# Kernel tuning notes

Hardware: AMD Instinct MI355X
Metric: run time of the kernel (lower is better)

The kernel has to match this reference:

```python
import jax, jax.numpy as jnp
import numpy as np

HEADS = 16
EPS = 1e-5

def _ln(t):
    # LayerNorm over last axis, no affine params
    mu = jnp.mean(t, axis=-1, keepdims=True)
    var = jnp.var(t, axis=-1, keepdims=True)
    return (t - mu) / jnp.sqrt(var + EPS)

def setup_inputs() -> dict:
    key = jax.random.key(0)
    ks = jax.random.split(key, 8)
    b, n, dim, mlp_dim = 4, 2048, 1024, 4096
    s = lambda d: 1.0 / np.sqrt(d)
    return {
        "x": jax.random.normal(ks[0], (b, n, dim), dtype=jnp.float32),
        "Wqkv": jax.random.uniform(ks[1], (dim, 3 * dim), jnp.float32, -s(dim), s(dim)),
        "W1": jax.random.uniform(ks[2], (dim, mlp_dim), jnp.float32, -s(dim), s(dim)),
        "b1": jax.random.uniform(ks[3], (mlp_dim,), jnp.float32, -s(dim), s(dim)),
        "W2": jax.random.uniform(ks[4], (mlp_dim, dim), jnp.float32, -s(mlp_dim), s(mlp_dim)),
        "b2": jax.random.uniform(ks[5], (dim,), jnp.float32, -s(mlp_dim), s(mlp_dim)),
        "Wout": jax.random.uniform(ks[6], (dim, dim), jnp.float32, -s(dim), s(dim)),
        "bout": jax.random.uniform(ks[7], (dim,), jnp.float32, -s(dim), s(dim)),
    }

def reference(x, Wqkv, W1, b1, W2, b2, Wout, bout):
    b, n, dim = x.shape
    h = HEADS
    d = dim // h
    scale = dim ** (-0.5)  # NOTE: module scales by full dim, not head_dim
    qkv = x @ Wqkv  # [b, n, 3*dim]
    qkv = qkv.reshape(b, n, 3, h, d).transpose(2, 0, 3, 1, 4)  # [3, b, h, n, d]
    q, k, v = qkv[0], qkv[1], qkv[2]
    q, k = _ln(q), _ln(k)
    dots = jnp.einsum('bhid,bhjd->bhij', q, k) * scale
    attn = jax.nn.softmax(dots, axis=-1)
    attn_v = jnp.einsum('bhij,bhjd->bhid', attn, v)
    attn_v = attn_v.transpose(0, 2, 1, 3).reshape(b, n, dim)
    attn_out = attn_v @ Wout + bout
    parallel = jax.nn.gelu(x @ W1 + b1, approximate=False) @ W2 + b2
    return _ln(attn_out + parallel)
```

## Files before the change

### kernel.cpp

```cpp
#include <hip/hip_runtime.h>

typedef __attribute__((ext_vector_type(8))) short s16x8;
typedef __attribute__((ext_vector_type(4))) short s16x4;
typedef __attribute__((ext_vector_type(4))) float f32x4;
typedef __attribute__((ext_vector_type(16))) float f32x16;
typedef __attribute__((ext_vector_type(2))) unsigned uint2v;

#define DEVINL __device__ __forceinline__

DEVINL float b2f(short u){ return __uint_as_float(((unsigned)(unsigned short)u) << 16); }
DEVINL short f2bf(float f){
  unsigned u = __float_as_uint(f);
  u += 0x7fffu + ((u >> 16) & 1u);
  return (short)(u >> 16);
}
DEVINL unsigned cvtpk(float lo, float hi){
  unsigned r;
  asm("v_cvt_pk_bf16_f32 %0, %1, %2" : "=v"(r) : "v"(lo), "v"(hi));
  return r;
}
DEVINL float max3f(float a, float b, float c){
  float r; asm("v_max3_f32 %0, %1, %2, %3" : "=v"(r) : "v"(a), "v"(b), "v"(c)); return r;
}

#if __has_builtin(__builtin_amdgcn_exp2f)
#define EXP2F __builtin_amdgcn_exp2f
#else
#define EXP2F exp2f
#endif

DEVINL f32x4 mfma32(s16x8 a, s16x8 b, f32x4 c){
  return __builtin_amdgcn_mfma_f32_16x16x32_bf16(a, b, c, 0, 0, 0);
}
DEVINL f32x16 mfma3216(s16x8 a, s16x8 b, f32x16 c){
  return __builtin_amdgcn_mfma_f32_32x32x16_bf16(a, b, c, 0, 0, 0);
}

DEVINL uint2v pl32swap(unsigned a, unsigned b){
#if __has_builtin(__builtin_amdgcn_permlane32_swap)
  return __builtin_amdgcn_permlane32_swap(a, b, false, false);
#else
  asm volatile("v_permlane32_swap_b32 %0, %1" : "+v"(a), "+v"(b));
  uint2v r; r[0] = a; r[1] = b; return r;
#endif
}

typedef const unsigned __attribute__((address_space(1)))* gas1;
typedef unsigned __attribute__((address_space(3)))* las3;
DEVINL void gload16(const short* g, short* l){
  __builtin_amdgcn_global_load_lds((gas1)g, (las3)l, 16, 0, 0);
}

#define CFENCE asm volatile("" ::: "memory")
#define PBAR  do{ CFENCE; __builtin_amdgcn_sched_barrier(0); __builtin_amdgcn_s_barrier(); \
                  __builtin_amdgcn_sched_barrier(0); CFENCE; }while(0)
#define VMW4 asm volatile("s_waitcnt vmcnt(4)" ::: "memory")
#define VMW3 asm volatile("s_waitcnt vmcnt(3)" ::: "memory")
#define VMW0 asm volatile("s_waitcnt vmcnt(0)" ::: "memory")
#define PRIO1 __builtin_amdgcn_s_setprio(1)
#define PRIO0 __builtin_amdgcn_s_setprio(0)

static const int Bc   = 4;
static const int Nc   = 2048;
static const int DIM  = 1024;
static const int Tc   = Bc * Nc;
static const int MLP  = 4096;
static const int D3   = 3072;

static const size_t OFF_XB    = 0;
static const size_t OFF_WQKVT = OFF_XB    + 16777216;
static const size_t OFF_W1T   = OFF_WQKVT + 6291456;
static const size_t OFF_W2T   = OFF_W1T   + 8388608;
static const size_t OFF_WOUTT = OFF_W2T   + 8388608;
static const size_t OFF_QKV   = OFF_WOUTT + 2097152;
static const size_t OFF_QLN   = OFF_QKV   + 50331648;
static const size_t OFF_KLN   = OFF_QLN   + 16777216;
static const size_t OFF_VT    = OFF_KLN   + 16777216;
static const size_t OFF_ATTNV = OFF_VT    + 16777216;
static const size_t OFF_H     = OFF_QKV;
static const size_t OFF_P2    = OFF_KLN;
static const size_t OFF_A2    = OFF_VT;

__global__ __launch_bounds__(256) void conv_x(const float* __restrict__ x, short* __restrict__ xb){
  size_t i = ((size_t)blockIdx.x * 256 + threadIdx.x) * 8;
  f32x4 v0 = *(const f32x4*)(x + i);
  f32x4 v1 = *(const f32x4*)(x + i + 4);
  s16x8 o;
#pragma unroll
  for (int j = 0; j < 4; ++j){ o[j] = f2bf(v0[j]); o[4+j] = f2bf(v1[j]); }
  *(s16x8*)(xb + i) = o;
}

__global__ __launch_bounds__(256) void transpose_conv(const float* __restrict__ W, short* __restrict__ Wt,
                                                      int K, int N){
  __shared__ float tile[32][33];
  int ntx = N >> 5;
  int tx = blockIdx.x % ntx, ty = blockIdx.x / ntx;
  int r = threadIdx.x >> 3, c = (threadIdx.x & 7) * 4;
  f32x4 v = *(const f32x4*)(W + (size_t)(ty*32 + r)*N + tx*32 + c);
  tile[r][c] = v[0]; tile[r][c+1] = v[1]; tile[r][c+2] = v[2]; tile[r][c+3] = v[3];
  __syncthreads();
  s16x4 o;
#pragma unroll
  for (int j = 0; j < 4; ++j) o[j] = f2bf(tile[c+j][r]);
  *(s16x4*)(Wt + (size_t)(tx*32 + r)*K + ty*32 + c) = o;
}

template<int BM, int ACT>
__global__ __launch_bounds__(512, 2) void gemmDP(const short* __restrict__ A, const short* __restrict__ Bt,
                                                 short* __restrict__ C, const float* __restrict__ bias,
                                                 int M, int N, int K){
  constexpr int MREP = BM/32;
  __shared__ short sA0[4096], sA1[4096], sA2[4096], sA3[4096];
  __shared__ short sA4[(BM==256)?4096:4], sA5[(BM==256)?4096:4];
  __shared__ short sA6[(BM==256)?4096:4], sA7[(BM==256)?4096:4];
  __shared__ short sB0[8192], sB1[8192], sB2[8192], sB3[8192];

  const int tid = threadIdx.x;
  const int w = tid >> 6, lane = tid & 63;
  const int lr = lane & 15, g = lane >> 4;
  const int wr = w >> 2, wc = w & 3;
  const int NT = K >> 6;
  const int NIT = NT >> 1;

  const int nbn = N >> 8;
  const int cpx = gridDim.x >> 3;
  const int bid = (int)blockIdx.x;
  const int sw = (bid & 7)*cpx + (bid >> 3);
  const int bm = sw / nbn, bn = sw % nbn;

  const int l2 = lane >> 2;
  const int gsw = ((lane & 3) - ((lane >> 3) & 3)) & 3;
  const int cof = gsw * 8;
  const int qsw8 = ((g + (lr >> 1)) & 3) * 8;

  const size_t arow = (BM==256) ? (size_t)(bm*256 + (w>>2)*128 + (w&3)*16 + l2)
                                : (size_t)(bm*128 + w*16 + l2);
  const short* ap0 = A  + arow*K + cof;
  const short* bp0 = Bt + (size_t)(bn*256 + w*16 + l2)*K + cof;

#define STA_(ARR, T, mh, kk) gload16(ap0 + (size_t)(mh)*64*K + (size_t)(T)*64 + (kk)*32, ARR + w*512)
#define STB_(ARR, T, kk) do{ gload16(bp0 + (size_t)(T)*64 + (kk)*32, ARR + w*512); \
                             gload16(bp0 + (size_t)128*K + (size_t)(T)*64 + (kk)*32, ARR + 4096 + w*512); }while(0)
#define LDA_(ARR, mi) (*(const s16x8*)&ARR[(wr*64 + (mi)*16 + lr)*32 + qsw8])
#define LDB_(ARR, ni) (*(const s16x8*)&ARR[(wc*64 + (ni)*16 + lr)*32 + qsw8])

  f32x4 acc[MREP][4] = {};

#define MMROW(ai, r) \
  acc[r][0]=mfma32(ai,b0,acc[r][0]); acc[r][1]=mfma32(ai,b1,acc[r][1]); \
  acc[r][2]=mfma32(ai,b2,acc[r][2]); acc[r][3]=mfma32(ai,b3,acc[r][3]);
#define RDA4(ARR) { a0=LDA_(ARR,0); a1=LDA_(ARR,1); a2=LDA_(ARR,2); a3=LDA_(ARR,3); }
#define RDB4(ARR) { b0=LDB_(ARR,0); b1=LDB_(ARR,1); b2=LDB_(ARR,2); b3=LDB_(ARR,3); }

  if constexpr (BM==256){
    STA_(sA0,0,0,0); STA_(sA1,0,1,0); STB_(sB0,0,0);
    STA_(sA2,0,0,1); STA_(sA3,0,1,1); STB_(sB1,0,1);
    STA_(sA4,1,0,0); STA_(sA5,1,1,0); STB_(sB2,1,0);
    VMW4;
  } else {
    STA_(sA0,0,0,0); STB_(sB0,0,0);
    STA_(sA1,0,0,1); STB_(sB1,0,1);
    STA_(sA2,1,0,0); STB_(sB2,1,0);
    VMW3;
  }
  PBAR;

  for (int i = 0; i < NIT; ++i){
    const int t = i << 1;
    const bool more = (t + 2 < NT);
    s16x8 a0,a1,a2,a3,b0,b1,b2,b3;

    if constexpr (BM==256){
      RDA4(sA0) RDB4(sB0)
      STA_(sA6, t+1, 0, 1); STA_(sA7, t+1, 1, 1);
      PBAR; PRIO1; MMROW(a0,0) MMROW(a1,1) MMROW(a2,2) MMROW(a3,3) PRIO0; PBAR;
      RDA4(sA1)
      STB_(sB3, t+1, 1);
      PBAR; PRIO1; MMROW(a0,4) MMROW(a1,5) MMROW(a2,6) MMROW(a3,7) PRIO0; PBAR;
      RDA4(sA2) RDB4(sB1)
      if (more){ STA_(sA0, t+2, 0, 0); STA_(sA1, t+2, 1, 0); }
      PBAR; PRIO1; MMROW(a0,0) MMROW(a1,1) MMROW(a2,2) MMROW(a3,3) PRIO0; PBAR;
      RDA4(sA3)
      if (more){ STB_(sB0, t+2, 0); }
      PBAR; PRIO1; MMROW(a0,4) MMROW(a1,5) MMROW(a2,6) MMROW(a3,7) PRIO0;
      if (more){ VMW4; } else { VMW0; }
      PBAR;
      RDA4(sA4) RDB4(sB2)
      if (more){ STA_(sA2, t+2, 0, 1); STA_(sA3, t+2, 1, 1); }
      PBAR; PRIO1; MMROW(a0,0) MMROW(a1,1) MMROW(a2,2) MMROW(a3,3) PRIO0; PBAR;
      RDA4(sA5)
      if (more){ STB_(sB1, t+2, 1); }
      PBAR; PRIO1; MMROW(a0,4) MMROW(a1,5) MMROW(a2,6) MMROW(a3,7) PRIO0; PBAR;
      RDA4(sA6) RDB4(sB3)
      if (more){ STA_(sA4, t+3, 0, 0); STA_(sA5, t+3, 1, 0); }
      PBAR; PRIO1; MMROW(a0,0) MMROW(a1,1) MMROW(a2,2) MMROW(a3,3) PRIO0; PBAR;
      RDA4(sA7)
      if (more){ STB_(sB2, t+3, 0); }
      PBAR; PRIO1; MMROW(a0,4) MMROW(a1,5) MMROW(a2,6) MMROW(a3,7) PRIO0;
      if (more){ VMW4; }
      PBAR;
    } else {
      RDA4(sA0) RDB4(sB0)
      STA_(sA3, t+1, 0, 1); STB_(sB3, t+1, 1);
      PBAR; PRIO1; MMROW(a0,0) MMROW(a1,1) MMROW(a2,2) MMROW(a3,3) PRIO0; PBAR;
      RDA4(sA1) RDB4(sB1)
      if (more){ STA_(sA0, t+2, 0, 0); STB_(sB0, t+2, 0); }
      PBAR; PRIO1; MMROW(a0,0) MMROW(a1,1) MMROW(a2,2) MMROW(a3,3) PRIO0;
      if (more){ VMW3; } else { VMW0; }
      PBAR;
      RDA4(sA2) RDB4(sB2)
      if (more){ STA_(sA1, t+2, 0, 1); STB_(sB1, t+2, 1); }
      PBAR; PRIO1; MMROW(a0,0) MMROW(a1,1) MMROW(a2,2) MMROW(a3,3) PRIO0; PBAR;
      RDA4(sA3) RDB4(sB3)
      if (more){ STA_(sA2, t+3, 0, 0); STB_(sB2, t+3, 0); }
      PBAR; PRIO1; MMROW(a0,0) MMROW(a1,1) MMROW(a2,2) MMROW(a3,3) PRIO0;
      if (more){ VMW3; }
      PBAR;
    }
  }
#undef MMROW
#undef RDA4
#undef RDB4
#undef STA_
#undef STB_
#undef LDA_
#undef LDB_

#pragma unroll
  for (int ni = 0; ni < 4; ++ni){
    const int col = bn*256 + wc*64 + ni*16 + lr;
    const float bv = bias ? bias[col] : 0.f;
#pragma unroll
    for (int a = 0; a < MREP; ++a){
      const int row0 = bm*BM + wr*(BM/2) + a*16 + 4*g;
      f32x4 v = acc[a][ni];
#pragma unroll
      for (int i = 0; i < 4; ++i){
        float val = v[i] + bv;
        if constexpr (ACT) val = 0.5f*val*(1.f + erff(val*0.70710678118f));
        C[(size_t)(row0+i)*N + col] = f2bf(val);
      }
    }
  }
}

__global__ __launch_bounds__(256) void ln_reorg(const short* __restrict__ qkv, short* __restrict__ qln,
                                                short* __restrict__ kln, short* __restrict__ vtb){
  __shared__ short vtile[64*72];
  int bh = blockIdx.x >> 5, tch = blockIdx.x & 31;
  int b = bh >> 4, h = bh & 15;
  int tq = threadIdx.x >> 2, j = threadIdx.x & 3;
  size_t row = (size_t)b*Nc + tch*64 + tq;
  const short* base = qkv + row*D3 + h*64 + j*16;
  size_t orow = ((size_t)bh*Nc + tch*64 + tq)*64 + j*16;

#pragma unroll
  for (int part = 0; part < 2; ++part){
    const short* src = base + part*DIM;
    s16x8 u0 = *(const s16x8*)src;
    s16x8 u1 = *(const s16x8*)(src + 8);
    float f[16]; float s = 0.f, sq = 0.f;
#pragma unroll
    for (int i = 0; i < 8; ++i){ f[i] = b2f(u0[i]); f[8+i] = b2f(u1[i]); }
#pragma unroll
    for (int i = 0; i < 16; ++i){ s += f[i]; sq += f[i]*f[i]; }
    s  += __shfl_xor(s, 1);  s  += __shfl_xor(s, 2);
    sq += __shfl_xor(sq, 1); sq += __shfl_xor(sq, 2);
    float mu = s * (1.f/64.f);
    float var = sq * (1.f/64.f) - mu*mu;
    float inv = rsqrtf(var + 1e-5f) * (part == 0 ? 0.04508422003f : 1.f);
    s16x8 o0, o1;
#pragma unroll
    for (int i = 0; i < 8; ++i){ o0[i] = f2bf((f[i]-mu)*inv); o1[i] = f2bf((f[8+i]-mu)*inv); }
    short* dst = (part == 0 ? qln : kln) + orow;
    *(s16x8*)dst = o0; *(s16x8*)(dst + 8) = o1;
  }

  s16x8 v0 = *(const s16x8*)(base + 2*DIM);
  s16x8 v1 = *(const s16x8*)(base + 2*DIM + 8);
  *(s16x8*)&vtile[tq*72 + j*16]     = v0;
  *(s16x8*)&vtile[tq*72 + j*16 + 8] = v1;
  __syncthreads();
  s16x8 o0, o1;
#pragma unroll
  for (int i = 0; i < 8; ++i){
    o0[i] = vtile[(j*16 + i)*72 + tq];
    o1[i] = vtile[(j*16 + 8 + i)*72 + tq];
  }
  short* vdst = vtb + ((size_t)bh*64 + tq)*Nc + tch*64 + j*16;
  *(s16x8*)vdst = o0; *(s16x8*)(vdst + 8) = o1;
}

__global__ __launch_bounds__(256) void attn_kern(const short* __restrict__ qln, const short* __restrict__ kln,
                                                 const short* __restrict__ vtb, short* __restrict__ attnv){
  __shared__ short Ks[128*72];
  __shared__ short Vs[64*136];
  const int tid = threadIdx.x;
  const int bh = blockIdx.x >> 4, qt = blockIdx.x & 15;
  const int b = bh >> 4, h = bh & 15;
  const int w = tid >> 6, lane = tid & 63;
  const int lq = lane & 31, hi = lane >> 5;
  const int qrow = qt*128 + w*32 + lq;

  const short* qp = qln + ((size_t)bh*Nc + qrow)*64 + hi*8;
  s16x8 qf[4];
#pragma unroll
  for (int m = 0; m < 4; ++m) qf[m] = *(const s16x8*)(qp + m*16);

  f32x16 o0 = {0,0,0,0,0,0,0,0,0,0,0,0,0,0,0,0};
  f32x16 o1 = {0,0,0,0,0,0,0,0,0,0,0,0,0,0,0,0};
  float mrun = -INFINITY, l = 0.f;

  const short* kb0 = kln + (size_t)bh*Nc*64;
  const short* vb0 = vtb + (size_t)bh*64*Nc;
  const int vrow = tid >> 2, vq = tid & 3;

  s16x8 kr[4], vr[4];
#pragma unroll
  for (int j = 0; j < 4; ++j){
    kr[j] = *(const s16x8*)(kb0 + (size_t)(tid + j*256)*8);
    vr[j] = *(const s16x8*)(vb0 + (size_t)vrow*Nc + (vq + 4*j)*8);
  }

  for (int kt = 0; kt < 16; ++kt){
#pragma unroll
    for (int j = 0; j < 4; ++j){
      int s = tid + j*256;
      *(s16x8*)&Ks[(s>>3)*72 + (s&7)*8] = kr[j];
      *(s16x8*)&Vs[vrow*136 + (vq + 4*j)*8] = vr[j];
    }
    __syncthreads();
    if (kt + 1 < 16){
      const short* kb = kb0 + (size_t)(kt+1)*128*64;
      const short* vb = vb0 + (kt+1)*128;
#pragma unroll
      for (int j = 0; j < 4; ++j){
        kr[j] = *(const s16x8*)(kb + (size_t)(tid + j*256)*8);
        vr[j] = *(const s16x8*)(vb + (size_t)vrow*Nc + (vq + 4*j)*8);
      }
    }

#pragma unroll
    for (int kc = 0; kc < 4; ++kc){
      f32x16 st = {0,0,0,0,0,0,0,0,0,0,0,0,0,0,0,0};
#pragma unroll
      for (int m = 0; m < 4; ++m){
        s16x8 kf = *(const s16x8*)&Ks[(kc*32 + lq)*72 + m*16 + hi*8];
        st = mfma3216(kf, qf[m], st);
      }
      float cmax = max3f(st[0], st[1], st[2]);
      cmax = max3f(cmax, st[3], st[4]);
      cmax = max3f(cmax, st[5], st[6]);
      cmax = max3f(cmax, st[7], st[8]);
      cmax = max3f(cmax, st[9], st[10]);
      cmax = max3f(cmax, st[11], st[12]);
      cmax = max3f(cmax, st[13], st[14]);
      cmax = fmaxf(cmax, st[15]);
      cmax = fmaxf(cmax, __shfl_xor(cmax, 32));
      if (__any(cmax > mrun + 8.f)){
        float mnew = fmaxf(mrun, cmax);
        float fr = EXP2F(mrun - mnew);
        l *= fr;
#pragma unroll
        for (int r = 0; r < 16; ++r){ o0[r] *= fr; o1[r] *= fr; }
        mrun = mnew;
      }
      float p[16];
#pragma unroll
      for (int r = 0; r < 16; ++r){ p[r] = EXP2F(st[r] - mrun); l += p[r]; }

#pragma unroll
      for (int kh = 0; kh < 2; ++kh){
        int r0 = kh*8;
        unsigned wa = cvtpk(p[r0+0], p[r0+1]);
        unsigned wb = cvtpk(p[r0+4], p[r0+5]);
        unsigned wc2 = cvtpk(p[r0+2], p[r0+3]);
        unsigned wd = cvtpk(p[r0+6], p[r0+7]);
        uint2v s1 = pl32swap(wa, wb);
        uint2v s2 = pl32swap(wc2, wd);
        union { unsigned u[4]; s16x8 v; } pu;
        pu.u[0] = s1[0]; pu.u[1] = s2[0]; pu.u[2] = s1[1]; pu.u[3] = s2[1];
        s16x8 vf0 = *(const s16x8*)&Vs[ lq      *136 + kc*32 + kh*16 + hi*8];
        s16x8 vf1 = *(const s16x8*)&Vs[(32 + lq)*136 + kc*32 + kh*16 + hi*8];
        o0 = mfma3216(vf0, pu.v, o0);
        o1 = mfma3216(vf1, pu.v, o1);
      }
    }
    __syncthreads();
  }

  l += __shfl_xor(l, 32);
  float inv = 1.f / l;
  short* orow = attnv + ((size_t)(b*Nc + qrow))*DIM + h*64;
#pragma unroll
  for (int r = 0; r < 16; r += 2){
    int dv = (r&3) + 8*(r>>2) + 4*hi;
    *(unsigned*)&orow[dv]      = cvtpk(o0[r]*inv, o0[r+1]*inv);
    *(unsigned*)&orow[32 + dv] = cvtpk(o1[r]*inv, o1[r+1]*inv);
  }
}

__global__ __launch_bounds__(256) void final_ln(const short* __restrict__ a2, const short* __restrict__ p2,
                                                float* __restrict__ out){
  __shared__ float red[16];
  int row = blockIdx.x, tid = threadIdx.x;
  size_t base = (size_t)row*DIM + tid*4;
  s16x4 a = *(const s16x4*)(a2 + base);
  s16x4 p = *(const s16x4*)(p2 + base);
  float v[4]; float s = 0.f, sq = 0.f;
#pragma unroll
  for (int i = 0; i < 4; ++i){ v[i] = b2f(a[i]) + b2f(p[i]); s += v[i]; sq += v[i]*v[i]; }
#pragma unroll
  for (int m = 1; m < 64; m <<= 1){ s += __shfl_xor(s, m); sq += __shfl_xor(sq, m); }
  int wv = tid >> 6;
  if ((tid & 63) == 0){ red[wv] = s; red[8 + wv] = sq; }
  __syncthreads();
  if (tid == 0){
    float S = red[0] + red[1] + red[2] + red[3];
    float Q = red[8] + red[9] + red[10] + red[11];
    float mu = S * (1.f/1024.f);
    float var = Q * (1.f/1024.f) - mu*mu;
    red[12] = mu; red[13] = rsqrtf(var + 1e-5f);
  }
  __syncthreads();
  float mu = red[12], inv = red[13];
#pragma unroll
  for (int i = 0; i < 4; ++i) out[base + i] = (v[i] - mu) * inv;
}

extern "C" void kernel_launch(void* const* d_in, const int* in_sizes, int n_in,
                              void* d_out, int out_size, void* d_ws, size_t ws_size,
                              hipStream_t stream){
  const float* x    = (const float*)d_in[0];
  const float* Wqkv = (const float*)d_in[1];
  const float* W1   = (const float*)d_in[2];
  const float* b1   = (const float*)d_in[3];
  const float* W2   = (const float*)d_in[4];
  const float* b2   = (const float*)d_in[5];
  const float* Wout = (const float*)d_in[6];
  const float* bout = (const float*)d_in[7];
  float* out = (float*)d_out;
  char* ws = (char*)d_ws;

  short* xb    = (short*)(ws + OFF_XB);
  short* wqkvt = (short*)(ws + OFF_WQKVT);
  short* w1t   = (short*)(ws + OFF_W1T);
  short* w2t   = (short*)(ws + OFF_W2T);
  short* woutt = (short*)(ws + OFF_WOUTT);
  short* qkv   = (short*)(ws + OFF_QKV);
  short* qln   = (short*)(ws + OFF_QLN);
  short* kln   = (short*)(ws + OFF_KLN);
  short* vtb   = (short*)(ws + OFF_VT);
  short* attnv = (short*)(ws + OFF_ATTNV);
  short* hbuf  = (short*)(ws + OFF_H);
  short* p2    = (short*)(ws + OFF_P2);
  short* a2    = (short*)(ws + OFF_A2);

  conv_x<<<4096, 256, 0, stream>>>(x, xb);
  transpose_conv<<<(DIM/32)*(D3/32),  256, 0, stream>>>(Wqkv, wqkvt, DIM, D3);
  transpose_conv<<<(DIM/32)*(MLP/32), 256, 0, stream>>>(W1, w1t, DIM, MLP);
  transpose_conv<<<(MLP/32)*(DIM/32), 256, 0, stream>>>(W2, w2t, MLP, DIM);
  transpose_conv<<<(DIM/32)*(DIM/32), 256, 0, stream>>>(Wout, woutt, DIM, DIM);

  gemmDP<128,0><<<(Tc/128)*(D3/256), 512, 0, stream>>>(xb, wqkvt, qkv, nullptr, Tc, D3, DIM);
  ln_reorg<<<64*32, 256, 0, stream>>>(qkv, qln, kln, vtb);
  attn_kern<<<64*16, 256, 0, stream>>>(qln, kln, vtb, attnv);

  gemmDP<256,1><<<(Tc/256)*(MLP/256), 512, 0, stream>>>(xb, w1t, hbuf, b1, Tc, MLP, DIM);
  gemmDP<128,0><<<(Tc/128)*(DIM/256), 512, 0, stream>>>(hbuf, w2t, p2, b2, Tc, DIM, MLP);
  gemmDP<128,0><<<(Tc/128)*(DIM/256), 512, 0, stream>>>(attnv, woutt, a2, bout, Tc, DIM, DIM);

  final_ln<<<Tc, 256, 0, stream>>>(a2, p2, out);
}
```

Measured before the change: 433.0 us.

## Replace GEMM with 128x128 four-wave kernel, grouped raster and LDS-staged stores

Replaces the 512-thread 128x256 and 256x256 GEMM kernels with a 256-thread 128x128 tile kernel using a unified four-stage LDS ring buffer. Block indices are remapped into 8x8 groups to improve L2 reuse of A and B. The epilogue writes through LDS so global stores become coalesced 16-byte rows instead of scattered 2-byte writes. Smaller tiles mean more blocks and higher occupancy, but less operand reuse per block and more total global traffic.

```diff
diff --git a/kernel.cpp b/kernel.cpp
--- a/kernel.cpp
+++ b/kernel.cpp
@@ -54,8 +54,8 @@
 #define CFENCE asm volatile("" ::: "memory")
 #define PBAR  do{ CFENCE; __builtin_amdgcn_sched_barrier(0); __builtin_amdgcn_s_barrier(); \
                   __builtin_amdgcn_sched_barrier(0); CFENCE; }while(0)
+#define VMW8 asm volatile("s_waitcnt vmcnt(8)" ::: "memory")
 #define VMW4 asm volatile("s_waitcnt vmcnt(4)" ::: "memory")
-#define VMW3 asm volatile("s_waitcnt vmcnt(3)" ::: "memory")
 #define VMW0 asm volatile("s_waitcnt vmcnt(0)" ::: "memory")
 #define PRIO1 __builtin_amdgcn_s_setprio(1)
 #define PRIO0 __builtin_amdgcn_s_setprio(0)
@@ -106,142 +106,120 @@
   *(s16x4*)(Wt + (size_t)(tx*32 + r)*K + ty*32 + c) = o;
 }
 
-template<int BM, int ACT>
-__global__ __launch_bounds__(512, 2) void gemmDP(const short* __restrict__ A, const short* __restrict__ Bt,
+template<int ACT>
+__global__ __launch_bounds__(256, 2) void gemmCF(const short* __restrict__ A, const short* __restrict__ Bt,
                                                  short* __restrict__ C, const float* __restrict__ bias,
                                                  int M, int N, int K){
-  constexpr int MREP = BM/32;
-  __shared__ short sA0[4096], sA1[4096], sA2[4096], sA3[4096];
-  __shared__ short sA4[(BM==256)?4096:4], sA5[(BM==256)?4096:4];
-  __shared__ short sA6[(BM==256)?4096:4], sA7[(BM==256)?4096:4];
-  __shared__ short sB0[8192], sB1[8192], sB2[8192], sB3[8192];
+  __shared__ short lds[32768];
 
   const int tid = threadIdx.x;
   const int w = tid >> 6, lane = tid & 63;
   const int lr = lane & 15, g = lane >> 4;
-  const int wr = w >> 2, wc = w & 3;
-  const int NT = K >> 6;
-  const int NIT = NT >> 1;
-
-  const int nbn = N >> 8;
+  const int wr = w >> 1, wc = w & 1;
+  const int NT = K >> 6, NIT = NT >> 1;
+
+  const int nbn = N >> 7;
   const int cpx = gridDim.x >> 3;
   const int bid = (int)blockIdx.x;
   const int sw = (bid & 7)*cpx + (bid >> 3);
-  const int bm = sw / nbn, bn = sw % nbn;
+  const int nbn8 = nbn >> 3;
+  const int T8 = sw >> 6, t64 = sw & 63;
+  const int bm = (T8 / nbn8)*8 + (t64 >> 3);
+  const int bn = (T8 % nbn8)*8 + (t64 & 7);
 
   const int l2 = lane >> 2;
   const int gsw = ((lane & 3) - ((lane >> 3) & 3)) & 3;
   const int cof = gsw * 8;
   const int qsw8 = ((g + (lr >> 1)) & 3) * 8;
 
-  const size_t arow = (BM==256) ? (size_t)(bm*256 + (w>>2)*128 + (w&3)*16 + l2)
-                                : (size_t)(bm*128 + w*16 + l2);
-  const short* ap0 = A  + arow*K + cof;
-  const short* bp0 = Bt + (size_t)(bn*256 + w*16 + l2)*K + cof;
-
-#define STA_(ARR, T, mh, kk) gload16(ap0 + (size_t)(mh)*64*K + (size_t)(T)*64 + (kk)*32, ARR + w*512)
-#define STB_(ARR, T, kk) do{ gload16(bp0 + (size_t)(T)*64 + (kk)*32, ARR + w*512); \
-                             gload16(bp0 + (size_t)128*K + (size_t)(T)*64 + (kk)*32, ARR + 4096 + w*512); }while(0)
-#define LDA_(ARR, mi) (*(const s16x8*)&ARR[(wr*64 + (mi)*16 + lr)*32 + qsw8])
-#define LDB_(ARR, ni) (*(const s16x8*)&ARR[(wc*64 + (ni)*16 + lr)*32 + qsw8])
-
-  f32x4 acc[MREP][4] = {};
-
-#define MMROW(ai, r) \
+  const short* ap0 = A  + (size_t)(bm*128 + w*16 + l2)*K + cof;
+  const short* bp0 = Bt + (size_t)(bn*128 + w*16 + l2)*K + cof;
+
+#define STG(soff, src, T_, kk) do{ \
+    gload16(src + (size_t)(T_)*64 + (kk)*32,                 lds + (soff) + w*512); \
+    gload16(src + (size_t)64*K + (size_t)(T_)*64 + (kk)*32,  lds + (soff) + 2048 + w*512); }while(0)
+#define STA(s, T_, kk) STG((s)*4096, ap0, T_, kk)
+#define STB(s, T_, kk) STG(16384 + (s)*4096, bp0, T_, kk)
+#define LDA(s, mi) (*(const s16x8*)&lds[(s)*4096 + (wr*64 + (mi)*16 + lr)*32 + qsw8])
+#define LDB(s, ni) (*(const s16x8*)&lds[16384 + (s)*4096 + (wc*64 + (ni)*16 + lr)*32 + qsw8])
+
+  f32x4 acc[4][4] = {};
+#define MM(ai, r) \
   acc[r][0]=mfma32(ai,b0,acc[r][0]); acc[r][1]=mfma32(ai,b1,acc[r][1]); \
   acc[r][2]=mfma32(ai,b2,acc[r][2]); acc[r][3]=mfma32(ai,b3,acc[r][3]);
-#define RDA4(ARR) { a0=LDA_(ARR,0); a1=LDA_(ARR,1); a2=LDA_(ARR,2); a3=LDA_(ARR,3); }
-#define RDB4(ARR) { b0=LDB_(ARR,0); b1=LDB_(ARR,1); b2=LDB_(ARR,2); b3=LDB_(ARR,3); }
-
-  if constexpr (BM==256){
-    STA_(sA0,0,0,0); STA_(sA1,0,1,0); STB_(sB0,0,0);
-    STA_(sA2,0,0,1); STA_(sA3,0,1,1); STB_(sB1,0,1);
-    STA_(sA4,1,0,0); STA_(sA5,1,1,0); STB_(sB2,1,0);
-    VMW4;
-  } else {
-    STA_(sA0,0,0,0); STB_(sB0,0,0);
-    STA_(sA1,0,0,1); STB_(sB1,0,1);
-    STA_(sA2,1,0,0); STB_(sB2,1,0);
-    VMW3;
-  }
+#define RD(s) s16x8 a0=LDA(s,0),a1=LDA(s,1),a2=LDA(s,2),a3=LDA(s,3), \
+                    b0=LDB(s,0),b1=LDB(s,1),b2=LDB(s,2),b3=LDB(s,3);
+#define MM16 MM(a0,0) MM(a1,1) MM(a2,2) MM(a3,3)
+
+  STA(0,0,0); STB(0,0,0);
+  STA(1,0,1); STB(1,0,1);
+  STA(2,1,0); STB(2,1,0);
+  VMW8;
   PBAR;
 
   for (int i = 0; i < NIT; ++i){
     const int t = i << 1;
-    const bool more = (t + 2 < NT);
-    s16x8 a0,a1,a2,a3,b0,b1,b2,b3;
-
-    if constexpr (BM==256){
-      RDA4(sA0) RDB4(sB0)
-      STA_(sA6, t+1, 0, 1); STA_(sA7, t+1, 1, 1);
-      PBAR; PRIO1; MMROW(a0,0) MMROW(a1,1) MMROW(a2,2) MMROW(a3,3) PRIO0; PBAR;
-      RDA4(sA1)
-      STB_(sB3, t+1, 1);
-      PBAR; PRIO1; MMROW(a0,4) MMROW(a1,5) MMROW(a2,6) MMROW(a3,7) PRIO0; PBAR;
-      RDA4(sA2) RDB4(sB1)
-      if (more){ STA_(sA0, t+2, 0, 0); STA_(sA1, t+2, 1, 0); }
-      PBAR; PRIO1; MMROW(a0,0) MMROW(a1,1) MMROW(a2,2) MMROW(a3,3) PRIO0; PBAR;
-      RDA4(sA3)
-      if (more){ STB_(sB0, t+2, 0); }
-      PBAR; PRIO1; MMROW(a0,4) MMROW(a1,5) MMROW(a2,6) MMROW(a3,7) PRIO0;
-      if (more){ VMW4; } else { VMW0; }
+    const bool more = (i + 1 < NIT);
+    {
+      RD(0)
+      STA(3, t+1, 1); STB(3, t+1, 1);
+      PBAR; PRIO1; MM16 PRIO0;
+      VMW8;
       PBAR;
-      RDA4(sA4) RDB4(sB2)
-      if (more){ STA_(sA2, t+2, 0, 1); STA_(sA3, t+2, 1, 1); }
-      PBAR; PRIO1; MMROW(a0,0) MMROW(a1,1) MMROW(a2,2) MMROW(a3,3) PRIO0; PBAR;
-      RDA4(sA5)
-      if (more){ STB_(sB1, t+2, 1); }
-      PBAR; PRIO1; MMROW(a0,4) MMROW(a1,5) MMROW(a2,6) MMROW(a3,7) PRIO0; PBAR;
-      RDA4(sA6) RDB4(sB3)
-      if (more){ STA_(sA4, t+3, 0, 0); STA_(sA5, t+3, 1, 0); }
-      PBAR; PRIO1; MMROW(a0,0) MMROW(a1,1) MMROW(a2,2) MMROW(a3,3) PRIO0; PBAR;
-      RDA4(sA7)
-      if (more){ STB_(sB2, t+3, 0); }
-      PBAR; PRIO1; MMROW(a0,4) MMROW(a1,5) MMROW(a2,6) MMROW(a3,7) PRIO0;
-      if (more){ VMW4; }
+    }
+    {
+      RD(1)
+      if (more){ STA(0, t+2, 0); STB(0, t+2, 0); }
+      PBAR; PRIO1; MM16 PRIO0;
+      if (more){ VMW8; } else { VMW4; }
       PBAR;
-    } else {
-      RDA4(sA0) RDB4(sB0)
-      STA_(sA3, t+1, 0, 1); STB_(sB3, t+1, 1);
-      PBAR; PRIO1; MMROW(a0,0) MMROW(a1,1) MMROW(a2,2) MMROW(a3,3) PRIO0; PBAR;
-      RDA4(sA1) RDB4(sB1)
-      if (more){ STA_(sA0, t+2, 0, 0); STB_(sB0, t+2, 0); }
-      PBAR; PRIO1; MMROW(a0,0) MMROW(a1,1) MMROW(a2,2) MMROW(a3,3) PRIO0;
-      if (more){ VMW3; } else { VMW0; }
+    }
+    {
+      RD(2)
+      if (more){ STA(1, t+2, 1); STB(1, t+2, 1); }
+      PBAR; PRIO1; MM16 PRIO0;
+      if (more){ VMW8; } else { VMW0; }
       PBAR;
-      RDA4(sA2) RDB4(sB2)
-      if (more){ STA_(sA1, t+2, 0, 1); STB_(sB1, t+2, 1); }
-      PBAR; PRIO1; MMROW(a0,0) MMROW(a1,1) MMROW(a2,2) MMROW(a3,3) PRIO0; PBAR;
-      RDA4(sA3) RDB4(sB3)
-      if (more){ STA_(sA2, t+3, 0, 0); STB_(sB2, t+3, 0); }
-      PBAR; PRIO1; MMROW(a0,0) MMROW(a1,1) MMROW(a2,2) MMROW(a3,3) PRIO0;
-      if (more){ VMW3; }
+    }
+    {
+      RD(3)
+      if (more){ STA(2, t+3, 0); STB(2, t+3, 0); }
+      PBAR; PRIO1; MM16 PRIO0;
+      if (more){ VMW8; }
       PBAR;
     }
   }
-#undef MMROW
-#undef RDA4
-#undef RDB4
-#undef STA_
-#undef STB_
-#undef LDA_
-#undef LDB_
-
-#pragma unroll
-  for (int ni = 0; ni < 4; ++ni){
-    const int col = bn*256 + wc*64 + ni*16 + lr;
-    const float bv = bias ? bias[col] : 0.f;
-#pragma unroll
-    for (int a = 0; a < MREP; ++a){
-      const int row0 = bm*BM + wr*(BM/2) + a*16 + 4*g;
+#undef MM
+#undef RD
+#undef MM16
+#undef STG
+#undef STA
+#undef STB
+#undef LDA
+#undef LDB
+
+#pragma unroll
+  for (int a = 0; a < 4; ++a){
+#pragma unroll
+    for (int ni = 0; ni < 4; ++ni){
+      const int col = wc*64 + ni*16 + lr;
+      const float bv = bias ? bias[bn*128 + col] : 0.f;
       f32x4 v = acc[a][ni];
 #pragma unroll
-      for (int i = 0; i < 4; ++i){
-        float val = v[i] + bv;
+      for (int ii = 0; ii < 4; ++ii){
+        float val = v[ii] + bv;
         if constexpr (ACT) val = 0.5f*val*(1.f + erff(val*0.70710678118f));
-        C[(size_t)(row0+i)*N + col] = f2bf(val);
+        lds[(wr*64 + a*16 + 4*g + ii)*128 + col] = f2bf(val);
       }
     }
+  }
+  __syncthreads();
+  const size_t crow0 = (size_t)bm * 128;
+  const int ch = (tid & 15) * 8;
+#pragma unroll
+  for (int p = 0; p < 8; ++p){
+    const int row = p*16 + (tid >> 4);
+    *(s16x8*)&C[(crow0 + row)*N + bn*128 + ch] = *(const s16x8*)&lds[row*128 + ch];
   }
 }
 
@@ -463,13 +441,13 @@
   transpose_conv<<<(MLP/32)*(DIM/32), 256, 0, stream>>>(W2, w2t, MLP, DIM);
   transpose_conv<<<(DIM/32)*(DIM/32), 256, 0, stream>>>(Wout, woutt, DIM, DIM);
 
-  gemmDP<128,0><<<(Tc/128)*(D3/256), 512, 0, stream>>>(xb, wqkvt, qkv, nullptr, Tc, D3, DIM);
+  gemmCF<0><<<(Tc/128)*(D3/128),  256, 0, stream>>>(xb, wqkvt, qkv, nullptr, Tc, D3, DIM);
   ln_reorg<<<64*32, 256, 0, stream>>>(qkv, qln, kln, vtb);
   attn_kern<<<64*16, 256, 0, stream>>>(qln, kln, vtb, attnv);
 
-  gemmDP<256,1><<<(Tc/256)*(MLP/256), 512, 0, stream>>>(xb, w1t, hbuf, b1, Tc, MLP, DIM);
-  gemmDP<128,0><<<(Tc/128)*(DIM/256), 512, 0, stream>>>(hbuf, w2t, p2, b2, Tc, DIM, MLP);
-  gemmDP<128,0><<<(Tc/128)*(DIM/256), 512, 0, stream>>>(attnv, woutt, a2, bout, Tc, DIM, DIM);
+  gemmCF<1><<<(Tc/128)*(MLP/128), 256, 0, stream>>>(xb, w1t, hbuf, b1, Tc, MLP, DIM);
+  gemmCF<0><<<(Tc/128)*(DIM/128), 256, 0, stream>>>(hbuf, w2t, p2, b2, Tc, DIM, MLP);
+  gemmCF<0><<<(Tc/128)*(DIM/128), 256, 0, stream>>>(attnv, woutt, a2, bout, Tc, DIM, DIM);
 
   final_ln<<<Tc, 256, 0, stream>>>(a2, p2, out);
 }
```

Measured after the change: 421.9 us. -2.6%, faster.
